# Kernel tuning notes

Hardware: AMD Instinct MI355X
Metric: run time of the kernel (lower is better)

## Reference

```python
import jax, jax.numpy as jnp
import numpy as np

B, N, D_IN, D_OUT, D_EDGE = 2, 512, 128, 128, 32
NEG_SLOPE = 0.2  # GATv2 LeakyReLU default


def _glorot(k, shape):
    lim = np.sqrt(6.0 / (shape[0] + shape[1]))
    return jax.random.uniform(k, shape, jnp.float32, -lim, lim)


def setup_inputs() -> dict:
    key = jax.random.key(0)
    ks = jax.random.split(key, 8)
    return {
        "node_features": jax.random.normal(ks[0], (B, N, D_IN), jnp.float32),
        "adj": jax.random.uniform(ks[1], (B, N, N)) < 0.1,  # sparse-ish dense adjacency
        "edge_features": jax.random.normal(ks[2], (B, N, N, D_EDGE), jnp.float32),
        "mask": jnp.ones((B, N), dtype=bool),
        "W_l": _glorot(ks[3], (D_IN, D_OUT)),   # source (lin_l)
        "b_l": jnp.zeros((D_OUT,), jnp.float32),
        "W_r": _glorot(ks[4], (D_IN, D_OUT)),   # target (lin_r)
        "b_r": jnp.zeros((D_OUT,), jnp.float32),
        "W_e": _glorot(ks[5], (D_EDGE, D_OUT)), # lin_edge (no bias)
        "att": _glorot(ks[6], (1, D_OUT))[0],   # attention vector [D_OUT]
        "bias": jnp.zeros((D_OUT,), jnp.float32),
    }


def _gatv2_dense(x, adj, e, mask, W_l, b_l, W_r, b_r, W_e, att, bias):
    # add self-loops (dense GAT convention)
    adj = adj | jnp.eye(N, dtype=bool)
    x_l = x @ W_l + b_l              # [B,N,D] source transform
    x_r = x @ W_r + b_r              # [B,N,D] target transform
    e_t = e @ W_e                    # [B,N,N,D] edge transform
    # edge (j -> i): pre[b,i,j,:] = x_l[b,j] + x_r[b,i] + e_t[b,i,j]
    pre = x_l[:, None, :, :] + x_r[:, :, None, :] + e_t
    score = jnp.einsum('bijd,d->bij', jax.nn.leaky_relu(pre, NEG_SLOPE), att)
    score = jnp.where(adj, score, -jnp.inf)
    alpha = jax.nn.softmax(score, axis=-1)  # softmax over neighbors j
    out = jnp.einsum('bij,bjd->bid', alpha, x_l) + bias
    return jnp.where(mask[:, :, None], out, 0.0)


def reference(node_features, adj, edge_features, mask, W_l, b_l, W_r, b_r, W_e, att, bias):
    return jax.nn.silu(
        _gatv2_dense(node_features, adj, edge_features, mask,
                     W_l, b_l, W_r, b_r, W_e, att, bias)
    )
```

## Files before the change

kernel.cpp:

```cpp
#include <hip/hip_runtime.h>
#include <math.h>

#define BATCH 2
#define NNODE 512
#define DIN   128
#define DOUT  128
#define DE    32
#define NEG   0.2f

typedef __attribute__((ext_vector_type(8))) short bf16x8;
typedef __attribute__((ext_vector_type(4))) float f32x4;

__device__ inline short f2bf(float f) {
    union { float f; unsigned u; } v; v.f = f;
    unsigned r = v.u + 0x7fffu + ((v.u >> 16) & 1u);
    return (short)(r >> 16);
}

__global__ __launch_bounds__(256) void xlr_kernel(
    const float* __restrict__ x,  const float* __restrict__ Wl,
    const float* __restrict__ bl, const float* __restrict__ Wr,
    const float* __restrict__ br, float* __restrict__ xl,
    float* __restrict__ xr)
{
    const int r0 = blockIdx.x * 4;
    const int d  = threadIdx.x & 127;
    const int hv = threadIdx.x >> 7;
    __shared__ float xs[4][DIN];
    for (int idx = threadIdx.x; idx < 4 * DIN; idx += 256)
        xs[idx >> 7][idx & 127] = x[(size_t)r0 * DIN + idx];
    __syncthreads();
    const int ra = 2 * hv, rb = ra + 1;
    float al0 = bl[d], al1 = al0, ar0 = br[d], ar1 = ar0;
    #pragma unroll 4
    for (int k = 0; k < DIN; ++k) {
        const float wl = Wl[k * DOUT + d], wr = Wr[k * DOUT + d];
        const float xa = xs[ra][k], xb = xs[rb][k];
        al0 = fmaf(xa, wl, al0); al1 = fmaf(xb, wl, al1);
        ar0 = fmaf(xa, wr, ar0); ar1 = fmaf(xb, wr, ar1);
    }
    xl[(size_t)(r0 + ra) * DOUT + d] = al0;
    xl[(size_t)(r0 + rb) * DOUT + d] = al1;
    xr[(size_t)(r0 + ra) * DOUT + d] = ar0;
    xr[(size_t)(r0 + rb) * DOUT + d] = ar1;
}

__global__ __launch_bounds__(256, 4) void gat_main(
    const float* __restrict__ xl, const float* __restrict__ xr,
    const void* __restrict__ adjv, const float* __restrict__ e,
    const void* __restrict__ maskv, const float* __restrict__ We,
    const float* __restrict__ att, const float* __restrict__ bias,
    float* __restrict__ out)
{
    const int bi   = blockIdx.x;
    const int b    = bi >> 9;
    const int i    = bi & (NNODE - 1);
    const int t    = threadIdx.x;
    const int wave = t >> 6;
    const int lane = t & 63;
    const int col  = lane & 15;
    const int g    = lane >> 4;

    __shared__ short WeT_s[DOUT][DE];
    __shared__ float att_s[DOUT];
    __shared__ float xr_s[DOUT];
    __shared__ float sc_s[NNODE];
    __shared__ float red_s[8];
    __shared__ float op_s[2][DOUT];
    __shared__ int   mflag[2];

    if (t < 2) mflag[t] = 0;
    for (int idx = t; idx < DE * DOUT; idx += 256) {
        const int k = idx >> 7, d = idx & 127;
        WeT_s[d][k] = f2bf(We[idx]);
    }
    if (t < DOUT) { att_s[t] = att[t]; xr_s[t] = xr[(size_t)bi * DOUT + t]; }
    __syncthreads();

    {
        const unsigned* aw = (const unsigned*)adjv;
        unsigned sawF = 0, sawG = 0;
        #pragma unroll
        for (int k = 0; k < 16; ++k) {
            const unsigned w = aw[t + 256 * k];
            sawF |= (w == 0x3f800000u);
            sawG |= (w > 1u);
        }
        if (sawF) atomicOr(&mflag[0], 1);
        if (sawG) atomicOr(&mflag[1], 1);
    }
    __syncthreads();
    const int byteMode = (!mflag[0] && mflag[1]) ? 1 : 0;

    const float* xlb = xl + (size_t)b * NNODE * DOUT;
    const float* eb  = e  + (size_t)bi * NNODE * DE;
    const unsigned char* adjB = (const unsigned char*)adjv + (size_t)bi * NNODE;
    const unsigned*      adjW = (const unsigned*)adjv + (size_t)bi * NNODE;

    bf16x8 bf[8];
    float  atv[8], xrv[8];
    #pragma unroll
    for (int dt = 0; dt < 8; ++dt) {
        bf[dt]  = *(const bf16x8*)&WeT_s[dt * 16 + col][g * 8];
        atv[dt] = att_s[dt * 16 + col];
        xrv[dt] = xr_s[dt * 16 + col];
    }

    for (int s = 0; s < 8; ++s) {
        const int jt = wave * 128 + s * 16;
        const float* ap = eb + (size_t)(jt + col) * DE + g * 8;
        const f32x4 a0 = *(const f32x4*)ap;
        const f32x4 a1 = *(const f32x4*)(ap + 4);
        bf16x8 af;
        af[0] = f2bf(a0[0]); af[1] = f2bf(a0[1]);
        af[2] = f2bf(a0[2]); af[3] = f2bf(a0[3]);
        af[4] = f2bf(a1[0]); af[5] = f2bf(a1[1]);
        af[6] = f2bf(a1[2]); af[7] = f2bf(a1[3]);

        f32x4 z = {0.f, 0.f, 0.f, 0.f};
        f32x4 c[8];
        #pragma unroll
        for (int dt = 0; dt < 8; ++dt)
            c[dt] = __builtin_amdgcn_mfma_f32_16x16x32_bf16(af, bf[dt], z, 0, 0, 0);

        float part[4] = {0.f, 0.f, 0.f, 0.f};
        #pragma unroll
        for (int dt = 0; dt < 8; ++dt) {
            const int d = dt * 16 + col;
            const float* xp = xlb + (size_t)(jt + g * 4) * DOUT + d;
            #pragma unroll
            for (int r = 0; r < 4; ++r) {
                float p = c[dt][r] + xrv[dt] + xp[(size_t)r * DOUT];
                p = p > 0.f ? p : NEG * p;
                part[r] = fmaf(atv[dt], p, part[r]);
            }
        }
        #pragma unroll
        for (int r = 0; r < 4; ++r) {
            part[r] += __shfl_xor(part[r], 1, 64);
            part[r] += __shfl_xor(part[r], 2, 64);
            part[r] += __shfl_xor(part[r], 4, 64);
            part[r] += __shfl_xor(part[r], 8, 64);
        }
        if (col == 0) {
            #pragma unroll
            for (int r = 0; r < 4; ++r) {
                const int j = jt + g * 4 + r;
                const bool conn = (j == i) ||
                    (byteMode ? (adjB[j] != 0) : (adjW[j] != 0));
                sc_s[j] = conn ? part[r] : -1e30f;
            }
        }
    }
    __syncthreads();

    float m = fmaxf(sc_s[t], sc_s[t + 256]);
    #pragma unroll
    for (int off = 32; off; off >>= 1) m = fmaxf(m, __shfl_xor(m, off, 64));
    if (lane == 0) red_s[wave] = m;
    __syncthreads();
    m = fmaxf(fmaxf(red_s[0], red_s[1]), fmaxf(red_s[2], red_s[3]));

    const float e0 = __expf(sc_s[t] - m);
    const float e1 = __expf(sc_s[t + 256] - m);
    sc_s[t] = e0; sc_s[t + 256] = e1;
    float ssum = e0 + e1;
    #pragma unroll
    for (int off = 32; off; off >>= 1) ssum += __shfl_xor(ssum, off, 64);
    if (lane == 0) red_s[4 + wave] = ssum;
    __syncthreads();
    const float inv = 1.f / (red_s[4] + red_s[5] + red_s[6] + red_s[7]);

    const int d = t & (DOUT - 1), hv = t >> 7;
    float acc = 0.f;
    const float* xlh  = xlb + (size_t)hv * 256 * DOUT;
    const float* wrow = sc_s + hv * 256;
    for (int j = 0; j < 256; ++j)
        acc = fmaf(wrow[j], xlh[(size_t)j * DOUT + d], acc);
    op_s[hv][d] = acc;
    __syncthreads();

    if (t < DOUT) {
        const bool mv = byteMode ? (((const unsigned char*)maskv)[bi] != 0)
                                 : (((const unsigned*)maskv)[bi] != 0);
        float v = (op_s[0][t] + op_s[1][t]) * inv + bias[t];
        if (!mv) v = 0.f;
        v = v / (1.f + __expf(-v));
        out[(size_t)bi * DOUT + t] = v;
    }
}

extern "C" void kernel_launch(void* const* d_in, const int* in_sizes, int n_in,
                              void* d_out, int out_size, void* d_ws, size_t ws_size,
                              hipStream_t stream)
{
    const float* x    = (const float*)d_in[0];
    const void*  adj  = d_in[1];
    const float* e    = (const float*)d_in[2];
    const void*  mask = d_in[3];
    const float* Wl   = (const float*)d_in[4];
    const float* bl   = (const float*)d_in[5];
    const float* Wr   = (const float*)d_in[6];
    const float* br   = (const float*)d_in[7];
    const float* We   = (const float*)d_in[8];
    const float* att  = (const float*)d_in[9];
    const float* bias = (const float*)d_in[10];
    float*       out  = (float*)d_out;

    float* xl = (float*)d_ws;
    float* xr = xl + (size_t)BATCH * NNODE * DOUT;

    xlr_kernel<<<(BATCH * NNODE) / 4, 256, 0, stream>>>(x, Wl, bl, Wr, br, xl, xr);
    gat_main<<<BATCH * NNODE, 256, 0, stream>>>(xl, xr, adj, e, mask, We,
                                                att, bias, out);
}
```

Baseline: 54.66 us.

## Split GAT into tiled score kernel and separate softmax-aggregation kernel

Replaces the one-block-per-target-node kernel with a 2D-tiled score kernel. Each block stages a 64-row x_l tile and a 16-row x_r tile in shared memory and reuses them across 16 target rows, then writes masked scores to a workspace. A separate aggregation kernel loads 8 score rows, does the softmax and the alpha·x_l product over a 64-column half, and applies bias, mask and SiLU. This cuts redundant global reads of x_l per target node and improves reuse, at the cost of an extra launch and a round-trip of the score matrix through global memory.

```diff
diff --git a/kernel.cpp b/kernel.cpp
--- a/kernel.cpp
+++ b/kernel.cpp
@@ -7,6 +7,9 @@
 #define DOUT  128
 #define DE    32
 #define NEG   0.2f
+#define TI    16
+#define TJ    64
+#define TIB   8
 
 typedef __attribute__((ext_vector_type(8))) short bf16x8;
 typedef __attribute__((ext_vector_type(4))) float f32x4;
@@ -45,16 +48,17 @@
     xr[(size_t)(r0 + rb) * DOUT + d] = ar1;
 }
 
-__global__ __launch_bounds__(256, 4) void gat_main(
+__global__ __launch_bounds__(256, 2) void score_kernel(
     const float* __restrict__ xl, const float* __restrict__ xr,
     const void* __restrict__ adjv, const float* __restrict__ e,
-    const void* __restrict__ maskv, const float* __restrict__ We,
-    const float* __restrict__ att, const float* __restrict__ bias,
-    float* __restrict__ out)
-{
-    const int bi   = blockIdx.x;
-    const int b    = bi >> 9;
-    const int i    = bi & (NNODE - 1);
+    const float* __restrict__ We, const float* __restrict__ att,
+    float* __restrict__ sc)
+{
+    const int bid = blockIdx.x;
+    const int jT  = bid & 7;
+    const int iT  = (bid >> 3) & 31;
+    const int b   = bid >> 8;
+    const int i0  = iT * TI, j0 = jT * TJ;
     const int t    = threadIdx.x;
     const int wave = t >> 6;
     const int lane = t & 63;
@@ -62,11 +66,9 @@
     const int g    = lane >> 4;
 
     __shared__ short WeT_s[DOUT][DE];
+    __shared__ float xl_s[TJ][DOUT + 4];
+    __shared__ float xr_s[TI][DOUT];
     __shared__ float att_s[DOUT];
-    __shared__ float xr_s[DOUT];
-    __shared__ float sc_s[NNODE];
-    __shared__ float red_s[8];
-    __shared__ float op_s[2][DOUT];
     __shared__ int   mflag[2];
 
     if (t < 2) mflag[t] = 0;
@@ -74,9 +76,15 @@
         const int k = idx >> 7, d = idx & 127;
         WeT_s[d][k] = f2bf(We[idx]);
     }
-    if (t < DOUT) { att_s[t] = att[t]; xr_s[t] = xr[(size_t)bi * DOUT + t]; }
-    __syncthreads();
-
+    for (int idx = t; idx < TJ * DOUT; idx += 256) {
+        const int jj = idx >> 7, d = idx & 127;
+        xl_s[jj][d] = xl[(size_t)(b * NNODE + j0 + jj) * DOUT + d];
+    }
+    for (int idx = t; idx < TI * DOUT; idx += 256) {
+        const int ii = idx >> 7, d = idx & 127;
+        xr_s[ii][d] = xr[(size_t)(b * NNODE + i0 + ii) * DOUT + d];
+    }
+    if (t < DOUT) att_s[t] = att[t];
     {
         const unsigned* aw = (const unsigned*)adjv;
         unsigned sawF = 0, sawG = 0;
@@ -92,23 +100,18 @@
     __syncthreads();
     const int byteMode = (!mflag[0] && mflag[1]) ? 1 : 0;
 
-    const float* xlb = xl + (size_t)b * NNODE * DOUT;
-    const float* eb  = e  + (size_t)bi * NNODE * DE;
-    const unsigned char* adjB = (const unsigned char*)adjv + (size_t)bi * NNODE;
-    const unsigned*      adjW = (const unsigned*)adjv + (size_t)bi * NNODE;
-
     bf16x8 bf[8];
-    float  atv[8], xrv[8];
+    float  atv[8];
     #pragma unroll
     for (int dt = 0; dt < 8; ++dt) {
         bf[dt]  = *(const bf16x8*)&WeT_s[dt * 16 + col][g * 8];
         atv[dt] = att_s[dt * 16 + col];
-        xrv[dt] = xr_s[dt * 16 + col];
-    }
-
-    for (int s = 0; s < 8; ++s) {
-        const int jt = wave * 128 + s * 16;
-        const float* ap = eb + (size_t)(jt + col) * DE + g * 8;
+    }
+
+    const int jw = j0 + wave * 16;
+    for (int i = 0; i < TI; ++i) {
+        const int ig = i0 + i;
+        const float* ap = e + ((size_t)(b * NNODE + ig) * NNODE + jw + col) * DE + g * 8;
         const f32x4 a0 = *(const f32x4*)ap;
         const f32x4 a1 = *(const f32x4*)(ap + 4);
         bf16x8 af;
@@ -127,10 +130,11 @@
         #pragma unroll
         for (int dt = 0; dt < 8; ++dt) {
             const int d = dt * 16 + col;
-            const float* xp = xlb + (size_t)(jt + g * 4) * DOUT + d;
+            const float xrv = xr_s[i][d];
             #pragma unroll
             for (int r = 0; r < 4; ++r) {
-                float p = c[dt][r] + xrv[dt] + xp[(size_t)r * DOUT];
+                const int jloc = wave * 16 + g * 4 + r;
+                float p = c[dt][r] + xrv + xl_s[jloc][d];
                 p = p > 0.f ? p : NEG * p;
                 part[r] = fmaf(atv[dt], p, part[r]);
             }
@@ -143,50 +147,108 @@
             part[r] += __shfl_xor(part[r], 8, 64);
         }
         if (col == 0) {
-            #pragma unroll
-            for (int r = 0; r < 4; ++r) {
-                const int j = jt + g * 4 + r;
-                const bool conn = (j == i) ||
-                    (byteMode ? (adjB[j] != 0) : (adjW[j] != 0));
-                sc_s[j] = conn ? part[r] : -1e30f;
+            const int jb = jw + g * 4;
+            const unsigned char* aB = (const unsigned char*)adjv + (size_t)(b * NNODE + ig) * NNODE;
+            const unsigned*      aW = (const unsigned*)adjv + (size_t)(b * NNODE + ig) * NNODE;
+            float4 v;
+            {
+                float* vp = (float*)&v;
+                #pragma unroll
+                for (int r = 0; r < 4; ++r) {
+                    const int j = jb + r;
+                    const bool conn = (j == ig) ||
+                        (byteMode ? (aB[j] != 0) : (aW[j] != 0));
+                    vp[r] = conn ? part[r] : -1e30f;
+                }
             }
-        }
+            *(float4*)&sc[(size_t)(b * NNODE + ig) * NNODE + jb] = v;
+        }
+    }
+}
+
+__global__ __launch_bounds__(256) void agg_kernel(
+    const float* __restrict__ xl, const float* __restrict__ sc,
+    const void* __restrict__ adjv, const void* __restrict__ maskv,
+    const float* __restrict__ bias, float* __restrict__ out)
+{
+    const int bid = blockIdx.x;
+    const int dh  = bid & 1;
+    const int iT  = (bid >> 1) & 63;
+    const int b   = bid >> 7;
+    const int i0  = iT * TIB, d0 = dh * 64;
+    const int t    = threadIdx.x;
+    const int wave = t >> 6;
+    const int lane = t & 63;
+
+    __shared__ float al_s[TIB][NNODE];
+    __shared__ int   mflag[2];
+
+    if (t < 2) mflag[t] = 0;
+    {
+        const unsigned* aw = (const unsigned*)adjv;
+        unsigned sawF = 0, sawG = 0;
+        #pragma unroll
+        for (int k = 0; k < 16; ++k) {
+            const unsigned w = aw[t + 256 * k];
+            sawF |= (w == 0x3f800000u);
+            sawG |= (w > 1u);
+        }
+        if (sawF) atomicOr(&mflag[0], 1);
+        if (sawG) atomicOr(&mflag[1], 1);
+    }
+    for (int idx = t; idx < TIB * NNODE; idx += 256) {
+        const int r = idx >> 9, jj = idx & 511;
+        al_s[r][jj] = sc[(size_t)(b * NNODE + i0 + r) * NNODE + jj];
     }
     __syncthreads();
-
-    float m = fmaxf(sc_s[t], sc_s[t + 256]);
+    const int byteMode = (!mflag[0] && mflag[1]) ? 1 : 0;
+
+    float invs[2];
     #pragma unroll
-    for (int off = 32; off; off >>= 1) m = fmaxf(m, __shfl_xor(m, off, 64));
-    if (lane == 0) red_s[wave] = m;
-    __syncthreads();
-    m = fmaxf(fmaxf(red_s[0], red_s[1]), fmaxf(red_s[2], red_s[3]));
-
-    const float e0 = __expf(sc_s[t] - m);
-    const float e1 = __expf(sc_s[t + 256] - m);
-    sc_s[t] = e0; sc_s[t + 256] = e1;
-    float ssum = e0 + e1;
+    for (int q = 0; q < 2; ++q) {
+        const int rr = wave + 4 * q;
+        float v[8], m = -1e30f;
+        #pragma unroll
+        for (int k = 0; k < 8; ++k) {
+            v[k] = al_s[rr][lane + 64 * k];
+            m = fmaxf(m, v[k]);
+        }
+        #pragma unroll
+        for (int off = 32; off; off >>= 1) m = fmaxf(m, __shfl_xor(m, off, 64));
+        float s = 0.f;
+        #pragma unroll
+        for (int k = 0; k < 8; ++k) {
+            const float ex = __expf(v[k] - m);
+            al_s[rr][lane + 64 * k] = ex;
+            s += ex;
+        }
+        #pragma unroll
+        for (int off = 32; off; off >>= 1) s += __shfl_xor(s, off, 64);
+        invs[q] = 1.f / s;
+    }
+
+    const int d = d0 + lane;
+    const float* xb = xl + (size_t)b * NNODE * DOUT + d;
+    float a0 = 0.f, a0b = 0.f, a1 = 0.f, a1b = 0.f;
+    for (int j = 0; j < NNODE; j += 2) {
+        const float x0 = xb[(size_t)j * DOUT];
+        const float x1 = xb[(size_t)(j + 1) * DOUT];
+        a0  = fmaf(al_s[wave][j],     x0, a0);
+        a0b = fmaf(al_s[wave][j + 1], x1, a0b);
+        a1  = fmaf(al_s[wave + 4][j],     x0, a1);
+        a1b = fmaf(al_s[wave + 4][j + 1], x1, a1b);
+    }
+    const float bv = bias[d];
     #pragma unroll
-    for (int off = 32; off; off >>= 1) ssum += __shfl_xor(ssum, off, 64);
-    if (lane == 0) red_s[4 + wave] = ssum;
-    __syncthreads();
-    const float inv = 1.f / (red_s[4] + red_s[5] + red_s[6] + red_s[7]);
-
-    const int d = t & (DOUT - 1), hv = t >> 7;
-    float acc = 0.f;
-    const float* xlh  = xlb + (size_t)hv * 256 * DOUT;
-    const float* wrow = sc_s + hv * 256;
-    for (int j = 0; j < 256; ++j)
-        acc = fmaf(wrow[j], xlh[(size_t)j * DOUT + d], acc);
-    op_s[hv][d] = acc;
-    __syncthreads();
-
-    if (t < DOUT) {
-        const bool mv = byteMode ? (((const unsigned char*)maskv)[bi] != 0)
-                                 : (((const unsigned*)maskv)[bi] != 0);
-        float v = (op_s[0][t] + op_s[1][t]) * inv + bias[t];
-        if (!mv) v = 0.f;
-        v = v / (1.f + __expf(-v));
-        out[(size_t)bi * DOUT + t] = v;
+    for (int q = 0; q < 2; ++q) {
+        const int row = i0 + wave + 4 * q;
+        const int mi  = b * NNODE + row;
+        const bool mv = byteMode ? (((const unsigned char*)maskv)[mi] != 0)
+                                 : (((const unsigned*)maskv)[mi] != 0);
+        float val = (q == 0 ? a0 + a0b : a1 + a1b) * invs[q] + bv;
+        if (!mv) val = 0.f;
+        val = val / (1.f + __expf(-val));
+        out[(size_t)mi * DOUT + d] = val;
     }
 }
 
@@ -209,8 +271,11 @@
 
     float* xl = (float*)d_ws;
     float* xr = xl + (size_t)BATCH * NNODE * DOUT;
+    float* sc = xr + (size_t)BATCH * NNODE * DOUT;
 
     xlr_kernel<<<(BATCH * NNODE) / 4, 256, 0, stream>>>(x, Wl, bl, Wr, br, xl, xr);
-    gat_main<<<BATCH * NNODE, 256, 0, stream>>>(xl, xr, adj, e, mask, We,
-                                                att, bias, out);
-}
+    score_kernel<<<BATCH * (NNODE / TI) * (NNODE / TJ), 256, 0, stream>>>(
+        xl, xr, adj, e, We, att, sc);
+    agg_kernel<<<BATCH * (NNODE / TIB) * 2, 256, 0, stream>>>(
+        xl, sc, adj, mask, bias, out);
+}
```

New measurement: 74.16 us. 35.7% more time.
